# Performance work log

Measured on AMD Instinct MI355X. Metric: run time of the kernel, lower is better.

The kernel has to match this reference:

```python
import jax, jax.numpy as jnp
import numpy as np
import math

CW = 10
T_S = 2.0


def _K(t0):
    t = t0 - CW // 2
    if t < 0:
        return -0.5 * math.exp(t / (T_S / 2.0))
    return math.exp(-t / T_S)

K_VALS = np.array([_K(k) for k in range(CW)], dtype=np.float32)          # synaptic kernel
KS_VALS = np.array([math.exp(-k / T_S) for k in range(CW)], dtype=np.float32)  # spike kernel


def swish(v):
    # original Swish: x * sigmoid(10*x)
    return v * jax.nn.sigmoid(10.0 * v)


def act_fun(v):
    # smooth surrogate spike activation: sigmoid(10*(mem - 0.5)), thresh=0.5
    return jax.nn.sigmoid(10.0 * (v - 0.5))


def setup_inputs() -> dict:
    key = jax.random.key(0)
    k1, k2, k3, k4 = jax.random.split(key, 4)
    B, T = 4096, 50
    x = jax.random.uniform(k1, (B, T, 620), dtype=jnp.float32)
    W1 = jax.random.normal(k2, (200, 620), dtype=jnp.float32) / np.sqrt(620.0)
    W2 = jax.random.normal(k3, (100, 200), dtype=jnp.float32) / np.sqrt(200.0)
    W3 = jax.random.normal(k4, (11, 100), dtype=jnp.float32) / np.sqrt(100.0)
    return {"x": x, "W1": W1, "W2": W2, "W3": W3}


def reference(x, W1, W2, W3):
    B, T, _ = x.shape
    kv = jnp.asarray(K_VALS)
    ks_tail = jnp.asarray(KS_VALS[1:])   # k=1..9; k=0 spike term is always 0 (buffer not yet written)
    kv_tail = jnp.asarray(K_VALS[1:])    # k=1..9 for layer-input history

    # h1 is purely feedforward in time -> precompute, then causal conv with K over CW window.
    h1 = swish(jnp.einsum('btd,nd->btn', x, W1))            # [B, T, 200]
    h1_pad = jnp.pad(h1, ((0, 0), (CW - 1, 0), (0, 0)))
    syn2 = sum(kv[k] * h1_pad[:, CW - 1 - k: CW - 1 - k + T] for k in range(CW))  # [B, T, 200]

    def shift(hist, new):
        # hist[:, j] holds value at time t-1-j; prepend current value
        return jnp.concatenate([new[:, None], hist[:, :-1]], axis=1)

    def step(carry, syn2_t):
        sl2_h, h2_h, sl3_h, h3_h, sl4_h, acc = carry
        # layer 2
        mem2 = syn2_t - jnp.einsum('k,bkn->bn', ks_tail, sl2_h)
        s2 = act_fun(mem2)
        sl2 = s2 * mem2
        h2 = swish(s2 @ W2.T)                                # [B, 100]
        # layer 3
        mem3 = kv[0] * h2 + jnp.einsum('k,bkn->bn', kv_tail, h2_h) \
               - jnp.einsum('k,bkn->bn', ks_tail, sl3_h)
        s3 = act_fun(mem3)
        sl3 = s3 * mem3
        h3 = swish(s3 @ W3.T)                                # [B, 11]
        # layer 4 (output)
        mem4 = kv[0] * h3 + jnp.einsum('k,bkn->bn', kv_tail, h3_h) \
               - jnp.einsum('k,bkn->bn', ks_tail, sl4_h)
        s4 = act_fun(mem4)
        sl4 = s4 * mem4
        carry = (shift(sl2_h, sl2), shift(h2_h, h2), shift(sl3_h, sl3),
                 shift(h3_h, h3), shift(sl4_h, sl4), acc + s4)
        return carry, None

    z = lambda n: jnp.zeros((B, CW - 1, n), dtype=x.dtype)
    carry0 = (z(200), z(100), z(100), z(11), z(11), jnp.zeros((B, 11), dtype=x.dtype))
    carry, _ = jax.lax.scan(step, carry0, jnp.swapaxes(syn2, 0, 1))
    h4_sumspike = carry[-1]
    return h4_sumspike / 50.0
```

## Files before the change

kernel.cpp:

```cpp
#include <hip/hip_runtime.h>
#include <math.h>

#define T_STEPS 50
#define D_IN    620
#define N1      200
#define N2      100
#define N3      11
#define BATCH   4096

typedef short bf16x8 __attribute__((ext_vector_type(8)));
typedef float f32x4  __attribute__((ext_vector_type(4)));

__device__ __constant__ float KV[10] = {
    -0.0033689735f, -0.0091578194f, -0.0248935342f, -0.0676676416f, -0.1839397206f,
     1.0f,           0.6065306597f,  0.3678794412f,  0.2231301601f,  0.1353352832f };

#define RHO    0.60653066f
#define RHO5   0.0820849986f
#define RHO10  0.0067379470f
#define KV0    (-0.0033689735f)
#define C1     (-0.0091578194f)
#define C2     (-0.0248935342f)
#define C3     (-0.0676676416f)
#define C4     (-0.1839397206f)

__device__ __forceinline__ float sigm10(float x) { return 1.0f / (1.0f + __expf(-10.0f * x)); }
__device__ __forceinline__ float swishf(float v) { return v / (1.0f + __expf(-10.0f * v)); }

__device__ __forceinline__ void split2(float x, unsigned short& hi, unsigned short& lo) {
    unsigned u = __float_as_uint(x);
    hi = (unsigned short)(u >> 16);
    float rem = x - __uint_as_float(u & 0xFFFF0000u);
    lo = (unsigned short)(__float_as_uint(rem) >> 16);
}

__global__ void prep_w1(const float* __restrict__ W1, unsigned short* __restrict__ W1pre) {
    int i = blockIdx.x * 256 + threadIdx.x;
    if (i >= 266240) return;
    int kk = i & 31;
    int t1 = i >> 5;
    int n  = t1 % 208;
    int t2 = t1 / 208;
    int p  = t2 & 1;
    int kt = t2 >> 1;
    int k  = kt * 32 + kk;
    float w = (n < N1 && k < D_IN) ? W1[n * D_IN + k] : 0.0f;
    unsigned short hi, lo; split2(w, hi, lo);
    int gsw = (kk >> 3) ^ ((n >> 1) & 3);
    int idx = kt * 13312 + p * 6656 + n * 32 + gsw * 8 + (kk & 7);
    W1pre[idx] = p ? lo : hi;
}

__global__ void prep_w2(const float* __restrict__ W2, unsigned short* __restrict__ W2pre2) {
    int i = blockIdx.x * 256 + threadIdx.x;
    if (i >= 57344) return;
    int e  = i & 7;
    int r  = i >> 3;
    int l  = r & 63;
    int r2 = r >> 6;
    int p  = r2 & 1;
    int r3 = r2 >> 1;
    int ks = r3 % 7;
    int wv = r3 / 7;
    int n  = wv * 16 + (l & 15);
    int k  = ks * 32 + (l >> 4) * 8 + e;
    float v = (n < N2 && k < N1) ? W2[n * N1 + k] : 0.0f;
    unsigned short hi, lo; split2(v, hi, lo);
    W2pre2[i] = p ? lo : hi;
}

__global__ __launch_bounds__(512, 4) void gemm1_mfma(const float* __restrict__ x,
                                                     const unsigned short* __restrict__ W1pre,
                                                     float* __restrict__ h1) {
    __shared__ unsigned short Bs[3][13312];

    const int tid = threadIdx.x;
    const int w   = tid >> 6;
    const int l   = tid & 63;
    const int j   = l >> 4;
    const int r16 = l & 15;
    const long row0 = (long)blockIdx.x * 128;
    const float* arow = x + (row0 + w * 16 + r16) * D_IN;

    f32x4 acc[13];
#pragma unroll
    for (int nt = 0; nt < 13; ++nt) acc[nt] = (f32x4){0.f, 0.f, 0.f, 0.f};

    auto stageB = [&](int kt, int bb) {
        const unsigned short* src = W1pre + kt * 13312;
        unsigned short* dst = &Bs[bb][0];
#pragma unroll
        for (int it = 0; it < 3; ++it) {
            int ch = it * 512 + tid;
            __builtin_amdgcn_global_load_lds(
                (const __attribute__((address_space(1))) unsigned int*)(src + ch * 8),
                (__attribute__((address_space(3))) unsigned int*)(dst + ch * 8), 16, 0, 0);
        }
        if (tid < 128) {
            int ch = 1536 + tid;
            __builtin_amdgcn_global_load_lds(
                (const __attribute__((address_space(1))) unsigned int*)(src + ch * 8),
                (__attribute__((address_space(3))) unsigned int*)(dst + ch * 8), 16, 0, 0);
        }
    };

    auto loadA = [&](int kt, float* av) {
        const float* p = arow + kt * 32 + j * 8;
        const float4 u0 = *(const float4*)p;
        const float4 u1 = *(const float4*)(p + 4);
        av[0] = u0.x; av[1] = u0.y; av[2] = u0.z; av[3] = u0.w;
        av[4] = u1.x; av[5] = u1.y; av[6] = u1.z; av[7] = u1.w;
    };
    auto loadAtail = [&](float* av) {
        if (j == 0) {
            const float4 u0 = *(const float4*)(arow + 608);
            const float4 u1 = *(const float4*)(arow + 612);
            av[0] = u0.x; av[1] = u0.y; av[2] = u0.z; av[3] = u0.w;
            av[4] = u1.x; av[5] = u1.y; av[6] = u1.z; av[7] = u1.w;
        } else if (j == 1) {
            const float4 u0 = *(const float4*)(arow + 616);
            av[0] = u0.x; av[1] = u0.y; av[2] = u0.z; av[3] = u0.w;
            av[4] = 0.f; av[5] = 0.f; av[6] = 0.f; av[7] = 0.f;
        } else {
#pragma unroll
            for (int e = 0; e < 8; ++e) av[e] = 0.f;
        }
    };

    float av[2][8];
    stageB(0, 0);
    stageB(1, 1);
    loadA(0, av[0]);
    loadA(1, av[1]);
    asm volatile("s_waitcnt vmcnt(7)" ::: "memory");
    asm volatile("s_barrier" ::: "memory");

#pragma unroll 1
    for (int kt = 0; kt < 20; ++kt) {
        bf16x8 ah, al;
#pragma unroll
        for (int e = 0; e < 8; ++e) {
            unsigned short hi, lo; split2(av[kt & 1][e], hi, lo);
            ah[e] = (short)hi; al[e] = (short)lo;
        }
        if (kt < 18) {
            if (kt + 2 == 19) loadAtail(av[kt & 1]); else loadA(kt + 2, av[kt & 1]);
            stageB(kt + 2, (kt + 2) % 3);
        }
        const unsigned short* B = &Bs[kt % 3][0];
#pragma unroll
        for (int nt = 0; nt < 13; ++nt) {
            const int n  = nt * 16 + r16;
            const int gs = j ^ ((n >> 1) & 3);
            const bf16x8 bh = *(const bf16x8*)(B + n * 32 + gs * 8);
            const bf16x8 bl = *(const bf16x8*)(B + 6656 + n * 32 + gs * 8);
            acc[nt] = __builtin_amdgcn_mfma_f32_16x16x32_bf16(ah, bh, acc[nt], 0, 0, 0);
            acc[nt] = __builtin_amdgcn_mfma_f32_16x16x32_bf16(ah, bl, acc[nt], 0, 0, 0);
            acc[nt] = __builtin_amdgcn_mfma_f32_16x16x32_bf16(al, bh, acc[nt], 0, 0, 0);
        }
        if (kt < 18) {
            asm volatile("s_waitcnt vmcnt(5)" ::: "memory");
            asm volatile("s_barrier" ::: "memory");
        } else if (kt == 18) {
            asm volatile("s_waitcnt vmcnt(0)" ::: "memory");
            asm volatile("s_barrier" ::: "memory");
        }
    }

#pragma unroll
    for (int nt = 0; nt < 13; ++nt) {
        const int gcol = nt * 16 + r16;
        if (gcol < N1) {
            const long grow0 = row0 + w * 16 + j * 4;
#pragma unroll
            for (int q = 0; q < 4; ++q)
                h1[(grow0 + q) * N1 + gcol] = swishf(acc[nt][q]);
        }
    }
}

__global__ __launch_bounds__(256) void conv_k(float* __restrict__ buf) {
    __shared__ float h1s[T_STEPS * N1];
    const int b = blockIdx.x, tid = threadIdx.x;
    float* p = buf + (size_t)b * (T_STEPS * N1);
    for (int i = tid; i < T_STEPS * N1 / 4; i += 256)
        ((float4*)h1s)[i] = ((const float4*)p)[i];
    __syncthreads();
    for (int i = tid; i < T_STEPS * N1; i += 256) {
        int t = i / N1, n = i - t * N1;
        float s = 0.0f;
#pragma unroll
        for (int k = 0; k < 10; ++k)
            if (k <= t) s = fmaf(KV[k], h1s[(t - k) * N1 + n], s);
        p[i] = s;
    }
}

__global__ __launch_bounds__(512, 2) void snn_scan5(const float* __restrict__ syn2,
                                                    const unsigned short* __restrict__ W2pre2,
                                                    const float* __restrict__ W3,
                                                    float* __restrict__ out) {
    __shared__ __align__(16) unsigned short s2A[8192];
    __shared__ __align__(16) float h2buf[8][132];
    __shared__ __align__(16) float s3buf[8][104];
    __shared__ __align__(16) float W3s[N3 * N2];
    __shared__ __align__(16) float pbuf[8][4][12];

    const int tid = threadIdx.x;
    const int wv  = tid >> 6;
    const int l   = tid & 63;
    const int m16 = l & 15;
    const int j2  = l >> 4;
    const int g   = wv;
    const int c   = l;
    const long b  = (long)blockIdx.x * 8 + g;

    for (int i = tid; i < N3 * N2; i += 512) W3s[i] = W3[i];
    for (int i = tid; i < 8192; i += 512) s2A[i] = 0;

    bf16x8 bh[7], bl[7];
    {
        const unsigned short* wp = W2pre2 + wv * 7168 + l * 8;
#pragma unroll
        for (int ks = 0; ks < 7; ++ks) {
            bh[ks] = *(const bf16x8*)(wp + ks * 1024);
            bl[ks] = *(const bf16x8*)(wp + ks * 1024 + 512);
        }
    }

    const int NL2 = (c < 8)  ? 4 : 3;
    const int NL3 = (c < 36) ? 2 : 1;
    const int o4  = c % 11;
    const int p4  = c / 11;
    const int kbeg = (p4 == 0) ? 0 : (4 + 24 * p4);
    const int nf4  = (p4 == 0) ? 7 : 6;

    float sl2h[10][4] = {}; float Ssl2[4] = {};
    float h2h[10][2]  = {}; float Dd3[2]  = {};
    float sl3h[10][2] = {}; float Ssl3[2] = {};
    float h3h[10]     = {}; float Dd4 = 0.f;
    float sl4h[10]    = {}; float Ssl4 = 0.f;
    float accum       = 0.0f;

    const float* syn2b = syn2 + b * (T_STEPS * N1);
    float syn_nxt[4];
#pragma unroll
    for (int jj = 0; jj < 4; ++jj) syn_nxt[jj] = (jj < NL2) ? syn2b[c + 64 * jj] : 0.0f;

    __syncthreads();

#pragma unroll 1
    for (int tb = 0; tb < T_STEPS; tb += 10) {
#pragma unroll
        for (int u = 0; u < 10; ++u) {
            const int t   = tb + u;
            const int um1 = (u + 9) % 10;
            const int um2 = (u + 8) % 10;
            const int um3 = (u + 7) % 10;
            const int um4 = (u + 6) % 10;
            const int um5 = (u + 5) % 10;

            float syn_cur[4];
#pragma unroll
            for (int jj = 0; jj < 4; ++jj) syn_cur[jj] = syn_nxt[jj];
            if (t + 1 < T_STEPS) {
#pragma unroll
                for (int jj = 0; jj < 4; ++jj)
                    if (jj < NL2) syn_nxt[jj] = syn2b[(t + 1) * N1 + c + 64 * jj];
            }

#pragma unroll
            for (int jj = 0; jj < 4; ++jj) {
                if (jj < NL2) {
                    const int n = c + 64 * jj;
                    const float slp = sl2h[um1][jj];
                    const float slo = sl2h[u][jj];
                    Ssl2[jj] = RHO * (Ssl2[jj] + slp) - RHO10 * slo;
                    const float mem2 = syn_cur[jj] - Ssl2[jj];
                    const float s2   = sigm10(mem2 - 0.5f);
                    sl2h[u][jj] = s2 * mem2;
                    unsigned short hi, lo; split2(s2, hi, lo);
                    const int off = g * 256 + (((n >> 3) ^ (g & 7)) * 8) + (n & 7);
                    s2A[off]        = hi;
                    s2A[4096 + off] = lo;
                }
            }
            __syncthreads();

            {
                f32x4 a0 = (f32x4){0.f, 0.f, 0.f, 0.f};
                f32x4 a1 = (f32x4){0.f, 0.f, 0.f, 0.f};
                const int swz = m16 & 7;
#pragma unroll
                for (int ks = 0; ks < 7; ++ks) {
                    const int gr = (4 * ks + j2) ^ swz;
                    const bf16x8 ahv = *(const bf16x8*)&s2A[m16 * 256 + gr * 8];
                    const bf16x8 alv = *(const bf16x8*)&s2A[4096 + m16 * 256 + gr * 8];
                    if (ks & 1) {
                        a1 = __builtin_amdgcn_mfma_f32_16x16x32_bf16(ahv, bh[ks], a1, 0, 0, 0);
                        a1 = __builtin_amdgcn_mfma_f32_16x16x32_bf16(alv, bh[ks], a1, 0, 0, 0);
                        a1 = __builtin_amdgcn_mfma_f32_16x16x32_bf16(ahv, bl[ks], a1, 0, 0, 0);
                    } else {
                        a0 = __builtin_amdgcn_mfma_f32_16x16x32_bf16(ahv, bh[ks], a0, 0, 0, 0);
                        a0 = __builtin_amdgcn_mfma_f32_16x16x32_bf16(alv, bh[ks], a0, 0, 0, 0);
                        a0 = __builtin_amdgcn_mfma_f32_16x16x32_bf16(ahv, bl[ks], a0, 0, 0, 0);
                    }
                }
                const f32x4 a = a0 + a1;
                if (j2 < 2) {
#pragma unroll
                    for (int q = 0; q < 4; ++q)
                        h2buf[j2 * 4 + q][wv * 16 + m16] = swishf(a[q]);
                }
            }
            __syncthreads();

#pragma unroll
            for (int jj = 0; jj < 2; ++jj) {
                if (jj < NL3) {
                    const int m = c + 64 * jj;
                    const float hm = h2buf[g][m];
                    float gneg = C1 * h2h[um1][jj];
                    gneg = fmaf(C2, h2h[um2][jj], gneg);
                    gneg = fmaf(C3, h2h[um3][jj], gneg);
                    gneg = fmaf(C4, h2h[um4][jj], gneg);
                    Dd3[jj] = fmaf(RHO, Dd3[jj], h2h[um5][jj]);
                    Dd3[jj] = fmaf(-RHO5, h2h[u][jj], Dd3[jj]);
                    const float slp = sl3h[um1][jj];
                    const float slo = sl3h[u][jj];
                    Ssl3[jj] = RHO * (Ssl3[jj] + slp) - RHO10 * slo;
                    const float mem3 = fmaf(KV0, hm, gneg) + Dd3[jj] - Ssl3[jj];
                    const float s3   = sigm10(mem3 - 0.5f);
                    sl3h[u][jj] = s3 * mem3;
                    h2h[u][jj]  = hm;
                    s3buf[g][m] = s3;
                }
            }
            asm volatile("s_waitcnt lgkmcnt(0)" ::: "memory");
            __builtin_amdgcn_sched_barrier(0);

            if (c < 44) {
                float part = 0.0f;
#pragma unroll
                for (int i = 0; i < 7; ++i) {
                    if (i < nf4) {
                        const float4 sv  = *(const float4*)&s3buf[g][kbeg + 4 * i];
                        const float4 wv4 = *(const float4*)&W3s[o4 * N2 + kbeg + 4 * i];
                        part = fmaf(sv.x, wv4.x, part);
                        part = fmaf(sv.y, wv4.y, part);
                        part = fmaf(sv.z, wv4.z, part);
                        part = fmaf(sv.w, wv4.w, part);
                    }
                }
                pbuf[g][p4][o4] = part;
            }
            asm volatile("s_waitcnt lgkmcnt(0)" ::: "memory");
            __builtin_amdgcn_sched_barrier(0);

            if (c < N3) {
                const float a4 = pbuf[g][0][c] + pbuf[g][1][c] + pbuf[g][2][c] + pbuf[g][3][c];
                const float h3 = swishf(a4);
                float gneg = C1 * h3h[um1];
                gneg = fmaf(C2, h3h[um2], gneg);
                gneg = fmaf(C3, h3h[um3], gneg);
                gneg = fmaf(C4, h3h[um4], gneg);
                Dd4 = fmaf(RHO, Dd4, h3h[um5]);
                Dd4 = fmaf(-RHO5, h3h[u], Dd4);
                const float slp = sl4h[um1];
                const float slo = sl4h[u];
                Ssl4 = RHO * (Ssl4 + slp) - RHO10 * slo;
                const float mem4 = fmaf(KV0, h3, gneg) + Dd4 - Ssl4;
                const float s4   = sigm10(mem4 - 0.5f);
                sl4h[u] = s4 * mem4;
                h3h[u]  = h3;
                accum += s4;
            }
        }
    }

    if (c < N3) out[b * N3 + c] = accum * 0.02f;
}

extern "C" void kernel_launch(void* const* d_in, const int* in_sizes, int n_in,
                              void* d_out, int out_size, void* d_ws, size_t ws_size,
                              hipStream_t stream) {
    const float* x  = (const float*)d_in[0];
    const float* W1 = (const float*)d_in[1];
    const float* W2 = (const float*)d_in[2];
    const float* W3 = (const float*)d_in[3];
    float* out = (float*)d_out;

    float* buf = (float*)d_ws;
    unsigned short* W1pre  = (unsigned short*)(buf + (size_t)BATCH * T_STEPS * N1);
    unsigned short* W2pre2 = W1pre + 266240;

    prep_w1<<<1040, 256, 0, stream>>>(W1, W1pre);
    prep_w2<<<224, 256, 0, stream>>>(W2, W2pre2);
    gemm1_mfma<<<1600, 512, 0, stream>>>(x, W1pre, buf);
    conv_k<<<BATCH, 256, 0, stream>>>(buf);
    snn_scan5<<<BATCH / 8, 512, 0, stream>>>(buf, W2pre2, W3, out);
}
```

Measured before the change: 529.7 us.

## Merge weight prep kernels, spread B-tail loads across waves, use four MFMA accumulators

```diff
diff --git a/kernel.cpp b/kernel.cpp
--- a/kernel.cpp
+++ b/kernel.cpp
@@ -34,39 +34,40 @@
     lo = (unsigned short)(__float_as_uint(rem) >> 16);
 }
 
-__global__ void prep_w1(const float* __restrict__ W1, unsigned short* __restrict__ W1pre) {
+__global__ void prep_w(const float* __restrict__ W1, const float* __restrict__ W2,
+                       unsigned short* __restrict__ W1pre, unsigned short* __restrict__ W2pre2) {
     int i = blockIdx.x * 256 + threadIdx.x;
-    if (i >= 266240) return;
-    int kk = i & 31;
-    int t1 = i >> 5;
-    int n  = t1 % 208;
-    int t2 = t1 / 208;
-    int p  = t2 & 1;
-    int kt = t2 >> 1;
-    int k  = kt * 32 + kk;
-    float w = (n < N1 && k < D_IN) ? W1[n * D_IN + k] : 0.0f;
-    unsigned short hi, lo; split2(w, hi, lo);
-    int gsw = (kk >> 3) ^ ((n >> 1) & 3);
-    int idx = kt * 13312 + p * 6656 + n * 32 + gsw * 8 + (kk & 7);
-    W1pre[idx] = p ? lo : hi;
-}
-
-__global__ void prep_w2(const float* __restrict__ W2, unsigned short* __restrict__ W2pre2) {
-    int i = blockIdx.x * 256 + threadIdx.x;
-    if (i >= 57344) return;
-    int e  = i & 7;
-    int r  = i >> 3;
-    int l  = r & 63;
-    int r2 = r >> 6;
-    int p  = r2 & 1;
-    int r3 = r2 >> 1;
-    int ks = r3 % 7;
-    int wv = r3 / 7;
-    int n  = wv * 16 + (l & 15);
-    int k  = ks * 32 + (l >> 4) * 8 + e;
-    float v = (n < N2 && k < N1) ? W2[n * N1 + k] : 0.0f;
-    unsigned short hi, lo; split2(v, hi, lo);
-    W2pre2[i] = p ? lo : hi;
+    if (i < 266240) {
+        int kk = i & 31;
+        int t1 = i >> 5;
+        int n  = t1 % 208;
+        int t2 = t1 / 208;
+        int p  = t2 & 1;
+        int kt = t2 >> 1;
+        int k  = kt * 32 + kk;
+        float w = (n < N1 && k < D_IN) ? W1[n * D_IN + k] : 0.0f;
+        unsigned short hi, lo; split2(w, hi, lo);
+        int gsw = (kk >> 3) ^ ((n >> 1) & 3);
+        int idx = kt * 13312 + p * 6656 + n * 32 + gsw * 8 + (kk & 7);
+        W1pre[idx] = p ? lo : hi;
+    } else {
+        int i2 = i - 266240;
+        if (i2 < 57344) {
+            int e  = i2 & 7;
+            int r  = i2 >> 3;
+            int l  = r & 63;
+            int r2 = r >> 6;
+            int p  = r2 & 1;
+            int r3 = r2 >> 1;
+            int ks = r3 % 7;
+            int wv = r3 / 7;
+            int n  = wv * 16 + (l & 15);
+            int k  = ks * 32 + (l >> 4) * 8 + e;
+            float v = (n < N2 && k < N1) ? W2[n * N1 + k] : 0.0f;
+            unsigned short hi, lo; split2(v, hi, lo);
+            W2pre2[i2] = p ? lo : hi;
+        }
+    }
 }
 
 __global__ __launch_bounds__(512, 4) void gemm1_mfma(const float* __restrict__ x,
@@ -96,8 +97,8 @@
                 (const __attribute__((address_space(1))) unsigned int*)(src + ch * 8),
                 (__attribute__((address_space(3))) unsigned int*)(dst + ch * 8), 16, 0, 0);
         }
-        if (tid < 128) {
-            int ch = 1536 + tid;
+        if (l < 16) {
+            int ch = 1536 + w * 16 + l;
             __builtin_amdgcn_global_load_lds(
                 (const __attribute__((address_space(1))) unsigned int*)(src + ch * 8),
                 (__attribute__((address_space(3))) unsigned int*)(dst + ch * 8), 16, 0, 0);
@@ -132,7 +133,7 @@
     stageB(1, 1);
     loadA(0, av[0]);
     loadA(1, av[1]);
-    asm volatile("s_waitcnt vmcnt(7)" ::: "memory");
+    asm volatile("s_waitcnt vmcnt(8)" ::: "memory");
     asm volatile("s_barrier" ::: "memory");
 
 #pragma unroll 1
@@ -159,7 +160,7 @@
             acc[nt] = __builtin_amdgcn_mfma_f32_16x16x32_bf16(al, bh, acc[nt], 0, 0, 0);
         }
         if (kt < 18) {
-            asm volatile("s_waitcnt vmcnt(5)" ::: "memory");
+            asm volatile("s_waitcnt vmcnt(6)" ::: "memory");
             asm volatile("s_barrier" ::: "memory");
         } else if (kt == 18) {
             asm volatile("s_waitcnt vmcnt(0)" ::: "memory");
@@ -290,23 +291,34 @@
             {
                 f32x4 a0 = (f32x4){0.f, 0.f, 0.f, 0.f};
                 f32x4 a1 = (f32x4){0.f, 0.f, 0.f, 0.f};
+                f32x4 a2 = (f32x4){0.f, 0.f, 0.f, 0.f};
+                f32x4 a3 = (f32x4){0.f, 0.f, 0.f, 0.f};
                 const int swz = m16 & 7;
 #pragma unroll
                 for (int ks = 0; ks < 7; ++ks) {
                     const int gr = (4 * ks + j2) ^ swz;
                     const bf16x8 ahv = *(const bf16x8*)&s2A[m16 * 256 + gr * 8];
                     const bf16x8 alv = *(const bf16x8*)&s2A[4096 + m16 * 256 + gr * 8];
-                    if (ks & 1) {
-                        a1 = __builtin_amdgcn_mfma_f32_16x16x32_bf16(ahv, bh[ks], a1, 0, 0, 0);
-                        a1 = __builtin_amdgcn_mfma_f32_16x16x32_bf16(alv, bh[ks], a1, 0, 0, 0);
-                        a1 = __builtin_amdgcn_mfma_f32_16x16x32_bf16(ahv, bl[ks], a1, 0, 0, 0);
-                    } else {
-                        a0 = __builtin_amdgcn_mfma_f32_16x16x32_bf16(ahv, bh[ks], a0, 0, 0, 0);
-                        a0 = __builtin_amdgcn_mfma_f32_16x16x32_bf16(alv, bh[ks], a0, 0, 0, 0);
-                        a0 = __builtin_amdgcn_mfma_f32_16x16x32_bf16(ahv, bl[ks], a0, 0, 0, 0);
+                    switch ((3 * ks + 0) & 3) {
+                        case 0: a0 = __builtin_amdgcn_mfma_f32_16x16x32_bf16(ahv, bh[ks], a0, 0, 0, 0); break;
+                        case 1: a1 = __builtin_amdgcn_mfma_f32_16x16x32_bf16(ahv, bh[ks], a1, 0, 0, 0); break;
+                        case 2: a2 = __builtin_amdgcn_mfma_f32_16x16x32_bf16(ahv, bh[ks], a2, 0, 0, 0); break;
+                        default: a3 = __builtin_amdgcn_mfma_f32_16x16x32_bf16(ahv, bh[ks], a3, 0, 0, 0); break;
+                    }
+                    switch ((3 * ks + 1) & 3) {
+                        case 0: a0 = __builtin_amdgcn_mfma_f32_16x16x32_bf16(alv, bh[ks], a0, 0, 0, 0); break;
+                        case 1: a1 = __builtin_amdgcn_mfma_f32_16x16x32_bf16(alv, bh[ks], a1, 0, 0, 0); break;
+                        case 2: a2 = __builtin_amdgcn_mfma_f32_16x16x32_bf16(alv, bh[ks], a2, 0, 0, 0); break;
+                        default: a3 = __builtin_amdgcn_mfma_f32_16x16x32_bf16(alv, bh[ks], a3, 0, 0, 0); break;
+                    }
+                    switch ((3 * ks + 2) & 3) {
+                        case 0: a0 = __builtin_amdgcn_mfma_f32_16x16x32_bf16(ahv, bl[ks], a0, 0, 0, 0); break;
+                        case 1: a1 = __builtin_amdgcn_mfma_f32_16x16x32_bf16(ahv, bl[ks], a1, 0, 0, 0); break;
+                        case 2: a2 = __builtin_amdgcn_mfma_f32_16x16x32_bf16(ahv, bl[ks], a2, 0, 0, 0); break;
+                        default: a3 = __builtin_amdgcn_mfma_f32_16x16x32_bf16(ahv, bl[ks], a3, 0, 0, 0); break;
                     }
                 }
-                const f32x4 a = a0 + a1;
+                const f32x4 a = (a0 + a1) + (a2 + a3);
                 if (j2 < 2) {
 #pragma unroll
                     for (int q = 0; q < 4; ++q)
@@ -326,9 +338,7 @@
                     gneg = fmaf(C4, h2h[um4][jj], gneg);
                     Dd3[jj] = fmaf(RHO, Dd3[jj], h2h[um5][jj]);
                     Dd3[jj] = fmaf(-RHO5, h2h[u][jj], Dd3[jj]);
-                    const float slp = sl3h[um1][jj];
-                    const float slo = sl3h[u][jj];
-                    Ssl3[jj] = RHO * (Ssl3[jj] + slp) - RHO10 * slo;
+                    Ssl3[jj] = RHO * (Ssl3[jj] + sl3h[um1][jj]) - RHO10 * sl3h[u][jj];
                     const float mem3 = fmaf(KV0, hm, gneg) + Dd3[jj] - Ssl3[jj];
                     const float s3   = sigm10(mem3 - 0.5f);
                     sl3h[u][jj] = s3 * mem3;
@@ -366,9 +376,7 @@
                 gneg = fmaf(C4, h3h[um4], gneg);
                 Dd4 = fmaf(RHO, Dd4, h3h[um5]);
                 Dd4 = fmaf(-RHO5, h3h[u], Dd4);
-                const float slp = sl4h[um1];
-                const float slo = sl4h[u];
-                Ssl4 = RHO * (Ssl4 + slp) - RHO10 * slo;
+                Ssl4 = RHO * (Ssl4 + sl4h[um1]) - RHO10 * sl4h[u];
                 const float mem4 = fmaf(KV0, h3, gneg) + Dd4 - Ssl4;
                 const float s4   = sigm10(mem4 - 0.5f);
                 sl4h[u] = s4 * mem4;
@@ -394,8 +402,7 @@
     unsigned short* W1pre  = (unsigned short*)(buf + (size_t)BATCH * T_STEPS * N1);
     unsigned short* W2pre2 = W1pre + 266240;
 
-    prep_w1<<<1040, 256, 0, stream>>>(W1, W1pre);
-    prep_w2<<<224, 256, 0, stream>>>(W2, W2pre2);
+    prep_w<<<1264, 256, 0, stream>>>(W1, W2, W1pre, W2pre2);
     gemm1_mfma<<<1600, 512, 0, stream>>>(x, W1pre, buf);
     conv_k<<<BATCH, 256, 0, stream>>>(buf);
     snn_scan5<<<BATCH / 8, 512, 0, stream>>>(buf, W2pre2, W3, out);
```

Result: slower. 562.2 us (+6.1%).
